# Kernel optimization log

Hardware: AMD Instinct MI355X
Metric: run time of the kernel (lower is better)

Reference implementation:

```python
import jax, jax.numpy as jnp
import numpy as np

IN_FEATURES = 4096
OUT_FEATURES = 14336
GROUP_SIZE = 128
EPS = 1e-6


def setup_inputs() -> dict:
    key = jax.random.key(0)
    k1, k2, k3, k4 = jax.random.split(key, 4)
    num_groups = IN_FEATURES // GROUP_SIZE
    x = jax.random.normal(k1, (8, IN_FEATURES), dtype=jnp.float32)
    weights_uint8 = jax.random.randint(k2, (OUT_FEATURES, IN_FEATURES), 0, 256, dtype=jnp.int32)
    # per-(out_row, group) [scale, min_val]; scale small so dequant weights are O(1)
    scales_min_vals = jax.random.normal(k3, (OUT_FEATURES * num_groups, 2), dtype=jnp.float32) * 0.01
    norm_weights = jnp.ones((IN_FEATURES,), dtype=jnp.float32)
    bias = jax.random.normal(k4, (OUT_FEATURES,), dtype=jnp.float32)
    return {
        "x": x,
        "weights_uint8": weights_uint8,
        "scales_min_vals": scales_min_vals,
        "norm_weights": norm_weights,
        "bias": bias,
    }


def _dequantize(weights_uint8, scales_min_vals):
    out_f, in_f = weights_uint8.shape
    ng = in_f // GROUP_SIZE
    smv = scales_min_vals.reshape(out_f, ng, 2)  # [O, G, 2]
    wq = weights_uint8.reshape(out_f, ng, GROUP_SIZE).astype(jnp.float32)
    # RTN dequant: w = q * scale + min_val, per group
    w = wq * smv[..., 0:1] + smv[..., 1:2]
    return w.reshape(out_f, in_f)


def _rmsnorm(x, norm_weights):
    var = jnp.mean(x * x, axis=-1, keepdims=True)
    return x * jax.lax.rsqrt(var + EPS) * norm_weights


def reference(x, weights_uint8, scales_min_vals, norm_weights, bias):
    xn = _rmsnorm(x, norm_weights)               # [B, I]
    w = _dequantize(weights_uint8, scales_min_vals)  # [O, I]
    return jnp.einsum('bi,oi->bo', xn, w) + bias  # [B, O]
```

## Files before the change

kernel.cpp:

```cpp
#include <hip/hip_runtime.h>

#define IN_F 4096
#define OUT_F 14336
#define NG 32
#define NB 8
#define RPW 7
#define RPB 28
#define NBLK 512

typedef int v4i __attribute__((ext_vector_type(4)));

__global__ __launch_bounds__(1024) void rmsnorm_k(const float* __restrict__ x,
                                                  const float* __restrict__ nw,
                                                  float* __restrict__ xn) {
  const int b = blockIdx.x;
  const int t = threadIdx.x;
  float4 v = reinterpret_cast<const float4*>(x + b * IN_F)[t];
  float ss = v.x * v.x + v.y * v.y + v.z * v.z + v.w * v.w;
#pragma unroll
  for (int m = 1; m < 64; m <<= 1) ss += __shfl_xor(ss, m, 64);
  __shared__ float red[16];
  if ((t & 63) == 0) red[t >> 6] = ss;
  __syncthreads();
  float tot = 0.f;
#pragma unroll
  for (int i = 0; i < 16; ++i) tot += red[i];
  const float r = rsqrtf(tot * (1.0f / IN_F) + 1e-6f);
  float4 w = reinterpret_cast<const float4*>(nw)[t];
  float4 o;
  o.x = v.x * r * w.x;
  o.y = v.y * r * w.y;
  o.z = v.z * r * w.z;
  o.w = v.w * r * w.w;
  reinterpret_cast<float4*>(xn + b * IN_F)[t] = o;
}

__global__ __launch_bounds__(256, 2) void gemv_k(const int* __restrict__ W,
                                                 const float2* __restrict__ smv,
                                                 const float* __restrict__ xn,
                                                 const float* __restrict__ bias,
                                                 float* __restrict__ out) {
  const int t = threadIdx.x;
  const int lane = t & 63;
  const int wave = t >> 6;
  const int row0 = blockIdx.x * RPB + wave * RPW;

  float acc[RPW][NB];
#pragma unroll
  for (int rr = 0; rr < RPW; ++rr)
#pragma unroll
    for (int b = 0; b < NB; ++b) acc[rr][b] = 0.f;

  const int lcol = lane * 4;
  for (int k = 0; k < 16; ++k) {
    const int col = k * 256 + lcol;
    float4 xv[NB];
#pragma unroll
    for (int b = 0; b < NB; ++b)
      xv[b] = *reinterpret_cast<const float4*>(xn + b * IN_F + col);
    const int g = col >> 7;
#pragma unroll
    for (int rr = 0; rr < RPW; ++rr) {
      const int o = row0 + rr;
      const v4i q = __builtin_nontemporal_load(
          reinterpret_cast<const v4i*>(W + o * IN_F + col));
      const float2 sm = smv[o * NG + g];
      const float w0 = fmaf((float)q.x, sm.x, sm.y);
      const float w1 = fmaf((float)q.y, sm.x, sm.y);
      const float w2 = fmaf((float)q.z, sm.x, sm.y);
      const float w3 = fmaf((float)q.w, sm.x, sm.y);
#pragma unroll
      for (int b = 0; b < NB; ++b) {
        acc[rr][b] = fmaf(w0, xv[b].x, acc[rr][b]);
        acc[rr][b] = fmaf(w1, xv[b].y, acc[rr][b]);
        acc[rr][b] = fmaf(w2, xv[b].z, acc[rr][b]);
        acc[rr][b] = fmaf(w3, xv[b].w, acc[rr][b]);
      }
    }
  }

  __shared__ float p[64][225];
#pragma unroll
  for (int rr = 0; rr < RPW; ++rr)
#pragma unroll
    for (int b = 0; b < NB; ++b)
      p[lane][wave * (RPW * NB) + rr * NB + b] = acc[rr][b];
  __syncthreads();

  if (t < RPB * NB) {
    float s0 = 0.f, s1 = 0.f, s2 = 0.f, s3 = 0.f;
#pragma unroll
    for (int l = 0; l < 64; l += 4) {
      s0 += p[l + 0][t];
      s1 += p[l + 1][t];
      s2 += p[l + 2][t];
      s3 += p[l + 3][t];
    }
    const int r = t >> 3;
    const int b = t & 7;
    const int o = blockIdx.x * RPB + r;
    out[b * OUT_F + o] = (s0 + s1) + (s2 + s3) + bias[o];
  }
}

extern "C" void kernel_launch(void* const* d_in, const int* in_sizes, int n_in,
                              void* d_out, int out_size, void* d_ws, size_t ws_size,
                              hipStream_t stream) {
  const float* x = (const float*)d_in[0];
  const int* W = (const int*)d_in[1];
  const float2* smv = (const float2*)d_in[2];
  const float* nw = (const float*)d_in[3];
  const float* bias = (const float*)d_in[4];
  float* out = (float*)d_out;
  float* xn = (float*)d_ws;

  rmsnorm_k<<<NB, 1024, 0, stream>>>(x, nw, xn);
  gemv_k<<<NBLK, 256, 0, stream>>>(W, smv, xn, bias, out);
}
```

Before: 314.2 us.

## Fuse RMSNorm into dequant GEMV and batch weight loads per k-step

Drops the separate RMSNorm kernel: each GEMV block recomputes per-batch sum of squares from x (128 KB read per block), then normalizes x on the fly inside the k-loop. Weight and scale loads for all rows are hoisted ahead of the FMAs to raise memory-level parallelism. This saves a launch and the xn round trip, but adds redundant norm work in every block plus extra multiplies per k-step, and more registers.

```diff
diff --git a/kernel.cpp b/kernel.cpp
--- a/kernel.cpp
+++ b/kernel.cpp
@@ -10,40 +10,48 @@
 
 typedef int v4i __attribute__((ext_vector_type(4)));
 
-__global__ __launch_bounds__(1024) void rmsnorm_k(const float* __restrict__ x,
-                                                  const float* __restrict__ nw,
-                                                  float* __restrict__ xn) {
-  const int b = blockIdx.x;
-  const int t = threadIdx.x;
-  float4 v = reinterpret_cast<const float4*>(x + b * IN_F)[t];
-  float ss = v.x * v.x + v.y * v.y + v.z * v.z + v.w * v.w;
-#pragma unroll
-  for (int m = 1; m < 64; m <<= 1) ss += __shfl_xor(ss, m, 64);
-  __shared__ float red[16];
-  if ((t & 63) == 0) red[t >> 6] = ss;
-  __syncthreads();
-  float tot = 0.f;
-#pragma unroll
-  for (int i = 0; i < 16; ++i) tot += red[i];
-  const float r = rsqrtf(tot * (1.0f / IN_F) + 1e-6f);
-  float4 w = reinterpret_cast<const float4*>(nw)[t];
-  float4 o;
-  o.x = v.x * r * w.x;
-  o.y = v.y * r * w.y;
-  o.z = v.z * r * w.z;
-  o.w = v.w * r * w.w;
-  reinterpret_cast<float4*>(xn + b * IN_F)[t] = o;
-}
-
-__global__ __launch_bounds__(256, 2) void gemv_k(const int* __restrict__ W,
-                                                 const float2* __restrict__ smv,
-                                                 const float* __restrict__ xn,
-                                                 const float* __restrict__ bias,
-                                                 float* __restrict__ out) {
+__global__ __launch_bounds__(256, 2) void fused_gemv_k(
+    const float* __restrict__ x, const int* __restrict__ W,
+    const float2* __restrict__ smv, const float* __restrict__ nw,
+    const float* __restrict__ bias, float* __restrict__ out) {
   const int t = threadIdx.x;
   const int lane = t & 63;
   const int wave = t >> 6;
   const int row0 = blockIdx.x * RPB + wave * RPW;
+
+  __shared__ float red[4][NB];
+  __shared__ float p[64][225];
+
+  float r_[NB];
+  {
+    float ss[NB];
+#pragma unroll
+    for (int b = 0; b < NB; ++b) ss[b] = 0.f;
+#pragma unroll
+    for (int i = 0; i < 4; ++i) {
+      const int idx = i * 256 + t;
+#pragma unroll
+      for (int b = 0; b < NB; ++b) {
+        const float4 v = reinterpret_cast<const float4*>(x + b * IN_F)[idx];
+        ss[b] += v.x * v.x + v.y * v.y + v.z * v.z + v.w * v.w;
+      }
+    }
+#pragma unroll
+    for (int b = 0; b < NB; ++b) {
+#pragma unroll
+      for (int m = 1; m < 64; m <<= 1) ss[b] += __shfl_xor(ss[b], m, 64);
+    }
+    if (lane == 0) {
+#pragma unroll
+      for (int b = 0; b < NB; ++b) red[wave][b] = ss[b];
+    }
+    __syncthreads();
+#pragma unroll
+    for (int b = 0; b < NB; ++b)
+      r_[b] = rsqrtf((red[0][b] + red[1][b] + red[2][b] + red[3][b]) *
+                         (1.0f / IN_F) +
+                     1e-6f);
+  }
 
   float acc[RPW][NB];
 #pragma unroll
@@ -54,21 +62,36 @@
   const int lcol = lane * 4;
   for (int k = 0; k < 16; ++k) {
     const int col = k * 256 + lcol;
+
+    v4i q[RPW];
+#pragma unroll
+    for (int rr = 0; rr < RPW; ++rr)
+      q[rr] = __builtin_nontemporal_load(
+          reinterpret_cast<const v4i*>(W + (row0 + rr) * IN_F + col));
+
+    const int g = col >> 7;
+    float2 sm[RPW];
+#pragma unroll
+    for (int rr = 0; rr < RPW; ++rr) sm[rr] = smv[(row0 + rr) * NG + g];
+
+    const float4 wv = *reinterpret_cast<const float4*>(nw + col);
     float4 xv[NB];
 #pragma unroll
-    for (int b = 0; b < NB; ++b)
-      xv[b] = *reinterpret_cast<const float4*>(xn + b * IN_F + col);
-    const int g = col >> 7;
+    for (int b = 0; b < NB; ++b) {
+      const float4 v = *reinterpret_cast<const float4*>(x + b * IN_F + col);
+      const float rb = r_[b];
+      xv[b].x = v.x * rb * wv.x;
+      xv[b].y = v.y * rb * wv.y;
+      xv[b].z = v.z * rb * wv.z;
+      xv[b].w = v.w * rb * wv.w;
+    }
+
 #pragma unroll
     for (int rr = 0; rr < RPW; ++rr) {
-      const int o = row0 + rr;
-      const v4i q = __builtin_nontemporal_load(
-          reinterpret_cast<const v4i*>(W + o * IN_F + col));
-      const float2 sm = smv[o * NG + g];
-      const float w0 = fmaf((float)q.x, sm.x, sm.y);
-      const float w1 = fmaf((float)q.y, sm.x, sm.y);
-      const float w2 = fmaf((float)q.z, sm.x, sm.y);
-      const float w3 = fmaf((float)q.w, sm.x, sm.y);
+      const float w0 = fmaf((float)q[rr].x, sm[rr].x, sm[rr].y);
+      const float w1 = fmaf((float)q[rr].y, sm[rr].x, sm[rr].y);
+      const float w2 = fmaf((float)q[rr].z, sm[rr].x, sm[rr].y);
+      const float w3 = fmaf((float)q[rr].w, sm[rr].x, sm[rr].y);
 #pragma unroll
       for (int b = 0; b < NB; ++b) {
         acc[rr][b] = fmaf(w0, xv[b].x, acc[rr][b]);
@@ -79,7 +102,6 @@
     }
   }
 
-  __shared__ float p[64][225];
 #pragma unroll
   for (int rr = 0; rr < RPW; ++rr)
 #pragma unroll
@@ -104,16 +126,14 @@
 }
 
 extern "C" void kernel_launch(void* const* d_in, const int* in_sizes, int n_in,
-                              void* d_out, int out_size, void* d_ws, size_t ws_size,
-                              hipStream_t stream) {
+                              void* d_out, int out_size, void* d_ws,
+                              size_t ws_size, hipStream_t stream) {
   const float* x = (const float*)d_in[0];
   const int* W = (const int*)d_in[1];
   const float2* smv = (const float2*)d_in[2];
   const float* nw = (const float*)d_in[3];
   const float* bias = (const float*)d_in[4];
   float* out = (float*)d_out;
-  float* xn = (float*)d_ws;
 
-  rmsnorm_k<<<NB, 1024, 0, stream>>>(x, nw, xn);
-  gemv_k<<<NBLK, 256, 0, stream>>>(W, smv, xn, bias, out);
+  fused_gemv_k<<<NBLK, 256, 0, stream>>>(x, W, smv, nw, bias, out);
 }
```

New measurement: 313.6 us. No clear change (-0.2%).
